# Optimization experiments

Hardware: AMD Instinct MI355X
Metric: run time of the kernel (lower is better)

Reference implementation:

```python
import jax, jax.numpy as jnp
import numpy as np

B, C, IMG, PS, S, D, H, HD, L, OUT = 512, 3, 36, 6, 36, 768, 12, 64, 4, 256

def _pos_embedding(seq_len, dim):
    # NOTE: cos at even indices, sin at odd (as in the torch source)
    position = np.arange(seq_len, dtype=np.float32)[:, None]
    div = np.exp(np.arange(0, dim, 2, dtype=np.float32) * -(np.log(10000.0) / dim))
    emb = np.zeros((seq_len, dim), dtype=np.float32)
    emb[:, 0::2] = np.cos(position * div)
    emb[:, 1::2] = np.sin(position * div)
    return jnp.asarray(emb)

def setup_inputs():
    ks = jax.random.split(jax.random.key(0), 10)
    sc = lambda f: 1.0 / np.sqrt(f)
    return {
        'batch': jax.random.normal(ks[0], (B, C, IMG, IMG), jnp.float32),
        'W_patch': jax.random.normal(ks[1], (D, PS * PS), jnp.float32) * sc(PS * PS),
        'b_patch': jnp.zeros((D,), jnp.float32),
        'pos': _pos_embedding(S, D),
        'ln1_g': jnp.ones((L, D), jnp.float32),
        'ln1_b': jnp.zeros((L, D), jnp.float32),
        'Wq': jax.random.normal(ks[2], (L, H, HD, HD), jnp.float32) * sc(HD),
        'bq': jnp.zeros((L, H, HD), jnp.float32),
        'Wk': jax.random.normal(ks[3], (L, H, HD, HD), jnp.float32) * sc(HD),
        'bk': jnp.zeros((L, H, HD), jnp.float32),
        'Wv': jax.random.normal(ks[4], (L, H, HD, HD), jnp.float32) * sc(HD),
        'bv': jnp.zeros((L, H, HD), jnp.float32),
        'ln2_g': jnp.ones((L, D), jnp.float32),
        'ln2_b': jnp.zeros((L, D), jnp.float32),
        'W1': jax.random.normal(ks[5], (L, 2 * D, D), jnp.float32) * sc(D),
        'b1': jnp.zeros((L, 2 * D), jnp.float32),
        'W2': jax.random.normal(ks[6], (L, D, 2 * D), jnp.float32) * sc(2 * D),
        'b2': jnp.zeros((L, D), jnp.float32),
        'W_out': jax.random.normal(ks[7], (OUT, D), jnp.float32) * sc(D),
        'b_out': jnp.zeros((OUT,), jnp.float32),
    }

def _layernorm(x, g, b):
    m = jnp.mean(x, axis=-1, keepdims=True)
    v = jnp.mean((x - m) ** 2, axis=-1, keepdims=True)
    return (x - m) / jnp.sqrt(v + 1e-5) * g + b

def _forward(batch, W_patch, b_patch, pos, ln1_g, ln1_b, Wq, bq, Wk, bk, Wv, bv,
             ln2_g, ln2_b, W1, b1, W2, b2, W_out, b_out):
    b_, c_ = batch.shape[0], batch.shape[1]
    # patchify: (B,C,36,36) -> (B,C,36 patches,36 pixels), matching torch unfold+reshape
    p = batch.reshape(b_, c_, IMG // PS, PS, IMG // PS, PS)
    p = p.transpose(0, 1, 2, 4, 3, 5).reshape(b_, c_, S, PS * PS)
    z = p @ W_patch.T + b_patch + pos  # pos broadcasts over (B,C)
    scale = 1.0 / np.sqrt(HD)
    for l in range(L):
        # pre-LN then batched per-head attention (collapses the python loops)
        h = _layernorm(z, ln1_g[l], ln1_b[l]).reshape(b_, c_, S, H, HD)
        q = jnp.einsum('bcshd,hed->bcshe', h, Wq[l]) + bq[l]
        k = jnp.einsum('bcshd,hed->bcshe', h, Wk[l]) + bk[l]
        v = jnp.einsum('bcshd,hed->bcshe', h, Wv[l]) + bv[l]
        attn = jax.nn.softmax(jnp.einsum('bcshe,bcthe->bchst', q, k) * scale, axis=-1)
        o = jnp.einsum('bchst,bcthe->bcshe', attn, v).reshape(b_, c_, S, D)
        z = z + o
        z = _layernorm(z, ln2_g[l], ln2_b[l])
        z = z + (jax.nn.relu(z @ W1[l].T + b1[l]) @ W2[l].T + b2[l])
    return z @ W_out.T + b_out

def reference(batch, W_patch, b_patch, pos, ln1_g, ln1_b, Wq, bq, Wk, bk, Wv, bv,
              ln2_g, ln2_b, W1, b1, W2, b2, W_out, b_out):
    return _forward(batch, W_patch, b_patch, pos, ln1_g, ln1_b, Wq, bq, Wk, bk, Wv, bv,
                    ln2_g, ln2_b, W1, b1, W2, b2, W_out, b_out)
```

## Files before the change

### kernel.cpp

```cpp
#include <hip/hip_runtime.h>
#include <hip/hip_bf16.h>
#include <cstdint>
#include <cstddef>

typedef __bf16 bf16;
typedef bf16 bf16x8 __attribute__((ext_vector_type(8)));
typedef bf16 bf16x4 __attribute__((ext_vector_type(4)));
typedef float f32x4 __attribute__((ext_vector_type(4)));
typedef unsigned int u32;

#define GLD_LDS16(gptr, lptr)                                                        \
  __builtin_amdgcn_global_load_lds((const __attribute__((address_space(1))) u32*)(gptr), \
                                   (__attribute__((address_space(3))) u32*)(lptr), 16, 0, 0)

static constexpr int S = 36, D = 768, H = 12, HD = 64, DFF = 1536;
static constexpr int BC = 1536;
static constexpr int M = BC * S;
static constexpr int OUTD = 256;

__global__ __launch_bounds__(256) void f2b_kernel(const float* __restrict__ in,
                                                  bf16* __restrict__ out, int n4) {
  int i = blockIdx.x * 256 + threadIdx.x;
  if (i < n4) {
    float4 f = ((const float4*)in)[i];
    bf16x4 o = {(bf16)f.x, (bf16)f.y, (bf16)f.z, (bf16)f.w};
    ((bf16x4*)out)[i] = o;
  }
}

__global__ __launch_bounds__(256) void patch_embed(const float* __restrict__ batch,
                                                   const float* __restrict__ Wp,
                                                   const float* __restrict__ bp,
                                                   const float* __restrict__ pos,
                                                   float* __restrict__ z) {
  int bc = blockIdx.x, tid = threadIdx.x;
  __shared__ float p[36][40];
  for (int i = tid; i < 1296; i += 256) {
    float f = batch[(size_t)bc * 1296 + i];
    int row = i / 36, col = i - row * 36;
    p[(row / 6) * 6 + col / 6][(row % 6) * 6 + (col % 6)] = f;
  }
  __syncthreads();
  for (int c0 = 0; c0 < 768; c0 += 256) {
    int d = c0 + tid;
    float wr[36];
    const float4* wp4 = (const float4*)(Wp + (size_t)d * 36);
#pragma unroll
    for (int q = 0; q < 9; ++q) {
      float4 f = wp4[q];
      wr[q * 4] = f.x; wr[q * 4 + 1] = f.y; wr[q * 4 + 2] = f.z; wr[q * 4 + 3] = f.w;
    }
    float gb = bp[d];
    for (int s = 0; s < 36; ++s) {
      float acc = 0.f;
#pragma unroll
      for (int k = 0; k < 36; ++k) acc += p[s][k] * wr[k];
      z[((size_t)bc * 36 + s) * 768 + d] = acc + gb + pos[s * 768 + d];
    }
  }
}

__global__ __launch_bounds__(256) void ln_stats(const float* __restrict__ zin,
                                                float* __restrict__ stats) {
  int row = blockIdx.x * 4 + (threadIdx.x >> 6);
  int lane = threadIdx.x & 63;
  const float* zr = zin + (size_t)row * D;
  float x[12];
#pragma unroll
  for (int i = 0; i < 12; ++i) x[i] = zr[i * 64 + lane];
  float s = 0.f;
#pragma unroll
  for (int i = 0; i < 12; ++i) s += x[i];
#pragma unroll
  for (int off = 32; off >= 1; off >>= 1) s += __shfl_xor(s, off, 64);
  float m = s * (1.f / 768.f);
  float v = 0.f;
#pragma unroll
  for (int i = 0; i < 12; ++i) { float dd = x[i] - m; v += dd * dd; }
#pragma unroll
  for (int off = 32; off >= 1; off >>= 1) v += __shfl_xor(v, off, 64);
  v *= (1.f / 768.f);
  if (lane == 0) {
    stats[(size_t)row * 2] = m;
    stats[(size_t)row * 2 + 1] = rsqrtf(v + 1e-5f);
  }
}

__global__ __launch_bounds__(256) void ln_inplace(float* __restrict__ z,
                                                  const float* __restrict__ g,
                                                  const float* __restrict__ bt) {
  int row = blockIdx.x * 4 + (threadIdx.x >> 6);
  int lane = threadIdx.x & 63;
  float* zr = z + (size_t)row * D;
  float x[12];
#pragma unroll
  for (int i = 0; i < 12; ++i) x[i] = zr[i * 64 + lane];
  float s = 0.f;
#pragma unroll
  for (int i = 0; i < 12; ++i) s += x[i];
#pragma unroll
  for (int off = 32; off >= 1; off >>= 1) s += __shfl_xor(s, off, 64);
  float m = s * (1.f / 768.f);
  float v = 0.f;
#pragma unroll
  for (int i = 0; i < 12; ++i) { float dd = x[i] - m; v += dd * dd; }
#pragma unroll
  for (int off = 32; off >= 1; off >>= 1) v += __shfl_xor(v, off, 64);
  v *= (1.f / 768.f);
  float rstd = rsqrtf(v + 1e-5f);
#pragma unroll
  for (int i = 0; i < 12; ++i) {
    int d = i * 64 + lane;
    zr[d] = (x[i] - m) * rstd * g[d] + bt[d];
  }
}

__global__ __launch_bounds__(64) void attn_kernel(const float* __restrict__ zg,
                                                  const float* __restrict__ stats,
                                                  const float* __restrict__ g1,
                                                  const float* __restrict__ b1_,
                                                  const bf16* __restrict__ Wq,
                                                  const bf16* __restrict__ Wk,
                                                  const bf16* __restrict__ Wv,
                                                  const float* __restrict__ bq,
                                                  const float* __restrict__ bk,
                                                  const float* __restrict__ bv,
                                                  float* __restrict__ z) {
  int head = blockIdx.x;
  int bc = blockIdx.y;
  __shared__ __align__(16) bf16 hbuf[48 * 64];
  __shared__ __align__(16) bf16 qbuf[48 * 64];
  __shared__ __align__(16) bf16 kbuf[48 * 64];
  __shared__ __align__(16) bf16 vt[64 * 64];
  __shared__ __align__(16) bf16 pbuf[48 * 64];
  int lane = threadIdx.x;
  int lr = lane & 15, quad = lane >> 4;

  for (int s2 = 36; s2 < 48; ++s2) hbuf[s2 * 64 + lane] = (bf16)0.f;
  for (int i = lane; i < 64 * 16; i += 64) { int e = i >> 4, t = 48 + (i & 15); vt[e * 64 + t] = (bf16)0.f; }
  for (int i = lane; i < 48 * 16; i += 64) { int s2 = i >> 4, t = 48 + (i & 15); pbuf[s2 * 64 + t] = (bf16)0.f; }
  const float* zsrc = zg + ((size_t)bc * S) * D + head * HD;
  const float* st = stats + (size_t)bc * S * 2;
  float gv = g1[head * HD + lane], bvv = b1_[head * HD + lane];
  for (int s2 = 0; s2 < 36; ++s2) {
    float mm = st[s2 * 2], rr = st[s2 * 2 + 1];
    hbuf[s2 * 64 + lane] = (bf16)((zsrc[(size_t)s2 * D + lane] - mm) * rr * gv + bvv);
  }
  __syncthreads();

  const bf16* Wm[3] = {Wq + (size_t)head * 4096, Wk + (size_t)head * 4096, Wv + (size_t)head * 4096};
  const float* Bm[3] = {bq + head * 64, bk + head * 64, bv + head * 64};
  for (int p = 0; p < 3; ++p) {
    bf16x8 bfr[4][2];
#pragma unroll
    for (int nt = 0; nt < 4; ++nt)
#pragma unroll
      for (int kt = 0; kt < 2; ++kt)
        bfr[nt][kt] = *(const bf16x8*)(Wm[p] + (nt * 16 + lr) * 64 + kt * 32 + quad * 8);
#pragma unroll
    for (int mt = 0; mt < 3; ++mt) {
      f32x4 acc[4] = {};
#pragma unroll
      for (int kt = 0; kt < 2; ++kt) {
        bf16x8 a = *(const bf16x8*)&hbuf[(mt * 16 + lr) * 64 + kt * 32 + quad * 8];
#pragma unroll
        for (int nt = 0; nt < 4; ++nt)
          acc[nt] = __builtin_amdgcn_mfma_f32_16x16x32_bf16(a, bfr[nt][kt], acc[nt], 0, 0, 0);
      }
#pragma unroll
      for (int nt = 0; nt < 4; ++nt) {
        float bb = Bm[p][nt * 16 + lr];
#pragma unroll
        for (int r = 0; r < 4; ++r) {
          int s2 = mt * 16 + quad * 4 + r;
          int e = nt * 16 + lr;
          float val = acc[nt][r] + bb;
          if (p == 0) qbuf[s2 * 64 + e] = (bf16)val;
          else if (p == 1) kbuf[s2 * 64 + e] = (bf16)val;
          else vt[e * 64 + s2] = (bf16)val;
        }
      }
    }
  }
  __syncthreads();

  f32x4 sc[3][3];
#pragma unroll
  for (int mt = 0; mt < 3; ++mt)
#pragma unroll
    for (int nt = 0; nt < 3; ++nt) {
      f32x4 a = {};
#pragma unroll
      for (int kt = 0; kt < 2; ++kt) {
        bf16x8 af = *(const bf16x8*)&qbuf[(mt * 16 + lr) * 64 + kt * 32 + quad * 8];
        bf16x8 bf_ = *(const bf16x8*)&kbuf[(nt * 16 + lr) * 64 + kt * 32 + quad * 8];
        a = __builtin_amdgcn_mfma_f32_16x16x32_bf16(af, bf_, a, 0, 0, 0);
      }
      int t = nt * 16 + lr;
#pragma unroll
      for (int r = 0; r < 4; ++r) {
        float v = a[r] * 0.125f;
        if (t >= 36) v = -1e30f;
        sc[mt][nt][r] = v;
      }
    }
#pragma unroll
  for (int mt = 0; mt < 3; ++mt) {
    float mx[4], sum[4];
#pragma unroll
    for (int r = 0; r < 4; ++r)
      mx[r] = fmaxf(fmaxf(sc[mt][0][r], sc[mt][1][r]), sc[mt][2][r]);
#pragma unroll
    for (int r = 0; r < 4; ++r)
#pragma unroll
      for (int off = 8; off >= 1; off >>= 1) mx[r] = fmaxf(mx[r], __shfl_xor(mx[r], off, 64));
#pragma unroll
    for (int r = 0; r < 4; ++r) sum[r] = 0.f;
#pragma unroll
    for (int nt = 0; nt < 3; ++nt)
#pragma unroll
      for (int r = 0; r < 4; ++r) {
        float e = __expf(sc[mt][nt][r] - mx[r]);
        sc[mt][nt][r] = e;
        sum[r] += e;
      }
#pragma unroll
    for (int r = 0; r < 4; ++r)
#pragma unroll
      for (int off = 8; off >= 1; off >>= 1) sum[r] += __shfl_xor(sum[r], off, 64);
#pragma unroll
    for (int nt = 0; nt < 3; ++nt)
#pragma unroll
      for (int r = 0; r < 4; ++r) {
        int s2 = mt * 16 + quad * 4 + r;
        int t = nt * 16 + lr;
        pbuf[s2 * 64 + t] = (bf16)(sc[mt][nt][r] / sum[r]);
      }
  }
  __syncthreads();

#pragma unroll
  for (int mt = 0; mt < 3; ++mt) {
    f32x4 o[4] = {};
#pragma unroll
    for (int kt = 0; kt < 2; ++kt) {
      bf16x8 a = *(const bf16x8*)&pbuf[(mt * 16 + lr) * 64 + kt * 32 + quad * 8];
#pragma unroll
      for (int nt = 0; nt < 4; ++nt) {
        bf16x8 b = *(const bf16x8*)&vt[(nt * 16 + lr) * 64 + kt * 32 + quad * 8];
        o[nt] = __builtin_amdgcn_mfma_f32_16x16x32_bf16(a, b, o[nt], 0, 0, 0);
      }
    }
#pragma unroll
    for (int nt = 0; nt < 4; ++nt)
#pragma unroll
      for (int r = 0; r < 4; ++r) {
        int s2 = mt * 16 + quad * 4 + r;
        if (s2 < 36) {
          int e = nt * 16 + lr;
          size_t idx = ((size_t)bc * S + s2) * D + head * HD + e;
          z[idx] += o[nt][r];
        }
      }
  }
}

template <int N, int K, int MODE, int AF32>
__global__ __launch_bounds__(256) void gemm_bt(const void* __restrict__ A,
                                               const bf16* __restrict__ Bw,
                                               const float* __restrict__ bias,
                                               const float* __restrict__ res,
                                               void* __restrict__ outp) {
  constexpr int BK = 64;
  __shared__ __align__(16) bf16 As[128 * BK];
  __shared__ __align__(16) bf16 Bs[128 * BK];
  int tid = threadIdx.x;
  int bn = blockIdx.x, bm = blockIdx.y;
  const bf16* Abf = (const bf16*)A + (size_t)bm * 128 * K;
  const float* Af = (const float*)A + (size_t)bm * 128 * K;
  const bf16* Bb = Bw + (size_t)bn * 128 * K;
  int lane = tid & 63, wave = tid >> 6;
  int wm = (wave >> 1) * 64, wn = (wave & 1) * 64;
  int lr = lane & 15, quad = lane >> 4;
  f32x4 acc[4][4] = {};
  for (int k0 = 0; k0 < K; k0 += BK) {
    if (AF32) {
#pragma unroll
      for (int r = 0; r < 8; ++r) {
        int c = r * 256 + tid;
        int row = c >> 4, col4 = (c & 15) * 4;
        float4 f = *(const float4*)(Af + (size_t)row * K + k0 + col4);
        bf16x4 o = {(bf16)f.x, (bf16)f.y, (bf16)f.z, (bf16)f.w};
        *(bf16x4*)&As[row * BK + col4] = o;
      }
    } else {
#pragma unroll
      for (int r = 0; r < 4; ++r) {
        int c = r * 256 + tid;
        int row = c >> 3, col = (c & 7) * 8;
        GLD_LDS16(Abf + (size_t)row * K + k0 + col, &As[c * 8]);
      }
    }
#pragma unroll
    for (int r = 0; r < 4; ++r) {
      int c = r * 256 + tid;
      int row = c >> 3, col = (c & 7) * 8;
      GLD_LDS16(Bb + (size_t)row * K + k0 + col, &Bs[c * 8]);
    }
    __syncthreads();
#pragma unroll
    for (int kt = 0; kt < 2; ++kt) {
      bf16x8 af[4], bfr[4];
#pragma unroll
      for (int mt = 0; mt < 4; ++mt) af[mt] = *(const bf16x8*)&As[(wm + mt * 16 + lr) * BK + kt * 32 + quad * 8];
#pragma unroll
      for (int nt = 0; nt < 4; ++nt) bfr[nt] = *(const bf16x8*)&Bs[(wn + nt * 16 + lr) * BK + kt * 32 + quad * 8];
#pragma unroll
      for (int mt = 0; mt < 4; ++mt)
#pragma unroll
        for (int nt = 0; nt < 4; ++nt)
          acc[mt][nt] = __builtin_amdgcn_mfma_f32_16x16x32_bf16(af[mt], bfr[nt], acc[mt][nt], 0, 0, 0);
    }
    __syncthreads();
  }
  int row0 = bm * 128 + wm + quad * 4;
  int col0 = bn * 128 + wn + lr;
#pragma unroll
  for (int mt = 0; mt < 4; ++mt)
#pragma unroll
    for (int nt = 0; nt < 4; ++nt) {
      int col = col0 + nt * 16;
      float bv = bias[col];
#pragma unroll
      for (int r = 0; r < 4; ++r) {
        size_t idx = (size_t)(row0 + mt * 16 + r) * N + col;
        float v = acc[mt][nt][r] + bv;
        if (MODE == 0) ((bf16*)outp)[idx] = (bf16)fmaxf(v, 0.f);
        else if (MODE == 1) ((float*)outp)[idx] = v + res[idx];
        else ((float*)outp)[idx] = v;
      }
    }
}

extern "C" void kernel_launch(void* const* d_in, const int* in_sizes, int n_in,
                              void* d_out, int out_size, void* d_ws, size_t ws_size,
                              hipStream_t stream) {
  const float* batch   = (const float*)d_in[0];
  const float* W_patch = (const float*)d_in[1];
  const float* b_patch = (const float*)d_in[2];
  const float* pos     = (const float*)d_in[3];
  const float* ln1_g   = (const float*)d_in[4];
  const float* ln1_b   = (const float*)d_in[5];
  const float* Wq      = (const float*)d_in[6];
  const float* bq      = (const float*)d_in[7];
  const float* Wk      = (const float*)d_in[8];
  const float* bk      = (const float*)d_in[9];
  const float* Wv      = (const float*)d_in[10];
  const float* bv      = (const float*)d_in[11];
  const float* ln2_g   = (const float*)d_in[12];
  const float* ln2_b   = (const float*)d_in[13];
  const float* W1      = (const float*)d_in[14];
  const float* b1      = (const float*)d_in[15];
  const float* W2      = (const float*)d_in[16];
  const float* b2      = (const float*)d_in[17];
  const float* W_out   = (const float*)d_in[18];
  const float* b_out   = (const float*)d_in[19];
  float* out = (float*)d_out;

  char* ws = (char*)d_ws;
  size_t off = 0;
  float* z     = (float*)(ws + off); off += (size_t)M * D * 4;
  float* stats = (float*)(ws + off); off += (size_t)M * 2 * 4;
  bf16* wq_b = (bf16*)(ws + off);    off += (size_t)4 * H * 4096 * 2;
  bf16* wk_b = (bf16*)(ws + off);    off += (size_t)4 * H * 4096 * 2;
  bf16* wv_b = (bf16*)(ws + off);    off += (size_t)4 * H * 4096 * 2;
  bf16* w1_b = (bf16*)(ws + off);    off += (size_t)4 * DFF * D * 2;
  bf16* w2_b = (bf16*)(ws + off);    off += (size_t)4 * D * DFF * 2;
  bf16* wo_b = (bf16*)(ws + off);    off += (size_t)OUTD * D * 2;
  bf16* act  = (bf16*)(ws + off);

  size_t avail = ws_size > off ? ws_size - off : (size_t)0;
  long long rcl = (long long)(avail / ((size_t)DFF * 2));
  int rc = (rcl > (long long)M) ? M : (int)rcl;
  rc = (rc / 128) * 128;
  if (rc <= 0) rc = 128;

  f2b_kernel<<<192, 256, 0, stream>>>(Wq, wq_b, 49152);
  f2b_kernel<<<192, 256, 0, stream>>>(Wk, wk_b, 49152);
  f2b_kernel<<<192, 256, 0, stream>>>(Wv, wv_b, 49152);
  f2b_kernel<<<4608, 256, 0, stream>>>(W1, w1_b, 1179648);
  f2b_kernel<<<4608, 256, 0, stream>>>(W2, w2_b, 1179648);
  f2b_kernel<<<192, 256, 0, stream>>>(W_out, wo_b, 49152);

  patch_embed<<<BC, 256, 0, stream>>>(batch, W_patch, b_patch, pos, z);

  for (int l = 0; l < 4; ++l) {
    ln_stats<<<M / 4, 256, 0, stream>>>(z, stats);
    attn_kernel<<<dim3(H, BC), 64, 0, stream>>>(z, stats, ln1_g + l * D, ln1_b + l * D,
        wq_b + (size_t)l * H * 4096, wk_b + (size_t)l * H * 4096, wv_b + (size_t)l * H * 4096,
        bq + l * H * 64, bk + l * H * 64, bv + l * H * 64, z);
    ln_inplace<<<M / 4, 256, 0, stream>>>(z, ln2_g + l * D, ln2_b + l * D);
    for (int m0 = 0; m0 < M; m0 += rc) {
      int mr = (M - m0 < rc) ? (M - m0) : rc;
      gemm_bt<DFF, D, 0, 1><<<dim3(DFF / 128, mr / 128), 256, 0, stream>>>(
          z + (size_t)m0 * D, w1_b + (size_t)l * DFF * D, b1 + l * DFF, nullptr, act);
      gemm_bt<D, DFF, 1, 0><<<dim3(D / 128, mr / 128), 256, 0, stream>>>(
          act, w2_b + (size_t)l * D * DFF, b2 + l * D, z + (size_t)m0 * D, z + (size_t)m0 * D);
    }
  }

  gemm_bt<OUTD, D, 2, 1><<<dim3(OUTD / 128, M / 128), 256, 0, stream>>>(
      z, wo_b, b_out, nullptr, out);
}
```

Baseline: 4.019 ms.

## Load LN1 output straight into MFMA fragments and pad attention LDS buffers

The attention kernel now builds the layernormed A fragments for the QKV projection directly in registers using vectorized float4 global loads, instead of staging them through an LDS hbuf. Row strides of the LDS buffers are padded from 64 to 72 to reduce bank conflicts. The probability matrix reuses the Q buffer instead of a separate pbuf, which needs an extra barrier and cuts LDS use, allowing more blocks per CU. The risk is higher register pressure from holding the fragments and gamma/beta values.

```diff
diff --git a/kernel.cpp b/kernel.cpp
--- a/kernel.cpp
+++ b/kernel.cpp
@@ -128,25 +128,59 @@
                                                   float* __restrict__ z) {
   int head = blockIdx.x;
   int bc = blockIdx.y;
-  __shared__ __align__(16) bf16 hbuf[48 * 64];
-  __shared__ __align__(16) bf16 qbuf[48 * 64];
-  __shared__ __align__(16) bf16 kbuf[48 * 64];
-  __shared__ __align__(16) bf16 vt[64 * 64];
-  __shared__ __align__(16) bf16 pbuf[48 * 64];
+  __shared__ __align__(16) bf16 qb[48 * 72];
+  __shared__ __align__(16) bf16 kb[48 * 72];
+  __shared__ __align__(16) bf16 vt[64 * 72];
   int lane = threadIdx.x;
   int lr = lane & 15, quad = lane >> 4;
 
-  for (int s2 = 36; s2 < 48; ++s2) hbuf[s2 * 64 + lane] = (bf16)0.f;
-  for (int i = lane; i < 64 * 16; i += 64) { int e = i >> 4, t = 48 + (i & 15); vt[e * 64 + t] = (bf16)0.f; }
-  for (int i = lane; i < 48 * 16; i += 64) { int s2 = i >> 4, t = 48 + (i & 15); pbuf[s2 * 64 + t] = (bf16)0.f; }
+#pragma unroll
+  for (int t0 = 0; t0 < 16; ++t0) vt[lane * 72 + 48 + t0] = (bf16)0.f;
+
   const float* zsrc = zg + ((size_t)bc * S) * D + head * HD;
   const float* st = stats + (size_t)bc * S * 2;
-  float gv = g1[head * HD + lane], bvv = b1_[head * HD + lane];
-  for (int s2 = 0; s2 < 36; ++s2) {
-    float mm = st[s2 * 2], rr = st[s2 * 2 + 1];
-    hbuf[s2 * 64 + lane] = (bf16)((zsrc[(size_t)s2 * D + lane] - mm) * rr * gv + bvv);
-  }
-  __syncthreads();
+
+  float gv[2][8], bvv[2][8];
+#pragma unroll
+  for (int kt = 0; kt < 2; ++kt) {
+    int c0 = head * HD + kt * 32 + quad * 8;
+    float4 ga = *(const float4*)(g1 + c0);
+    float4 gb2 = *(const float4*)(g1 + c0 + 4);
+    float4 ba = *(const float4*)(b1_ + c0);
+    float4 bb2 = *(const float4*)(b1_ + c0 + 4);
+    gv[kt][0] = ga.x; gv[kt][1] = ga.y; gv[kt][2] = ga.z; gv[kt][3] = ga.w;
+    gv[kt][4] = gb2.x; gv[kt][5] = gb2.y; gv[kt][6] = gb2.z; gv[kt][7] = gb2.w;
+    bvv[kt][0] = ba.x; bvv[kt][1] = ba.y; bvv[kt][2] = ba.z; bvv[kt][3] = ba.w;
+    bvv[kt][4] = bb2.x; bvv[kt][5] = bb2.y; bvv[kt][6] = bb2.z; bvv[kt][7] = bb2.w;
+  }
+
+  bf16x8 hfrag[3][2];
+#pragma unroll
+  for (int mt = 0; mt < 3; ++mt) {
+    int srow = mt * 16 + lr;
+    if (srow < 36) {
+      float mm = st[srow * 2], rr = st[srow * 2 + 1];
+#pragma unroll
+      for (int kt = 0; kt < 2; ++kt) {
+        int c0 = kt * 32 + quad * 8;
+        float4 f0 = *(const float4*)(zsrc + (size_t)srow * D + c0);
+        float4 f1 = *(const float4*)(zsrc + (size_t)srow * D + c0 + 4);
+        float hv[8] = {f0.x, f0.y, f0.z, f0.w, f1.x, f1.y, f1.z, f1.w};
+        bf16x8 o;
+#pragma unroll
+        for (int j = 0; j < 8; ++j) o[j] = (bf16)((hv[j] - mm) * rr * gv[kt][j] + bvv[kt][j]);
+        hfrag[mt][kt] = o;
+      }
+    } else {
+#pragma unroll
+      for (int kt = 0; kt < 2; ++kt) {
+        bf16x8 o;
+#pragma unroll
+        for (int j = 0; j < 8; ++j) o[j] = (bf16)0.f;
+        hfrag[mt][kt] = o;
+      }
+    }
+  }
 
   const bf16* Wm[3] = {Wq + (size_t)head * 4096, Wk + (size_t)head * 4096, Wv + (size_t)head * 4096};
   const float* Bm[3] = {bq + head * 64, bk + head * 64, bv + head * 64};
@@ -161,12 +195,10 @@
     for (int mt = 0; mt < 3; ++mt) {
       f32x4 acc[4] = {};
 #pragma unroll
-      for (int kt = 0; kt < 2; ++kt) {
-        bf16x8 a = *(const bf16x8*)&hbuf[(mt * 16 + lr) * 64 + kt * 32 + quad * 8];
+      for (int kt = 0; kt < 2; ++kt)
 #pragma unroll
         for (int nt = 0; nt < 4; ++nt)
-          acc[nt] = __builtin_amdgcn_mfma_f32_16x16x32_bf16(a, bfr[nt][kt], acc[nt], 0, 0, 0);
-      }
+          acc[nt] = __builtin_amdgcn_mfma_f32_16x16x32_bf16(hfrag[mt][kt], bfr[nt][kt], acc[nt], 0, 0, 0);
 #pragma unroll
       for (int nt = 0; nt < 4; ++nt) {
         float bb = Bm[p][nt * 16 + lr];
@@ -175,9 +207,9 @@
           int s2 = mt * 16 + quad * 4 + r;
           int e = nt * 16 + lr;
           float val = acc[nt][r] + bb;
-          if (p == 0) qbuf[s2 * 64 + e] = (bf16)val;
-          else if (p == 1) kbuf[s2 * 64 + e] = (bf16)val;
-          else vt[e * 64 + s2] = (bf16)val;
+          if (p == 0) qb[s2 * 72 + e] = (bf16)val;
+          else if (p == 1) kb[s2 * 72 + e] = (bf16)val;
+          else vt[e * 72 + s2] = (bf16)val;
         }
       }
     }
@@ -192,8 +224,8 @@
       f32x4 a = {};
 #pragma unroll
       for (int kt = 0; kt < 2; ++kt) {
-        bf16x8 af = *(const bf16x8*)&qbuf[(mt * 16 + lr) * 64 + kt * 32 + quad * 8];
-        bf16x8 bf_ = *(const bf16x8*)&kbuf[(nt * 16 + lr) * 64 + kt * 32 + quad * 8];
+        bf16x8 af = *(const bf16x8*)&qb[(mt * 16 + lr) * 72 + kt * 32 + quad * 8];
+        bf16x8 bf_ = *(const bf16x8*)&kb[(nt * 16 + lr) * 72 + kt * 32 + quad * 8];
         a = __builtin_amdgcn_mfma_f32_16x16x32_bf16(af, bf_, a, 0, 0, 0);
       }
       int t = nt * 16 + lr;
@@ -204,6 +236,8 @@
         sc[mt][nt][r] = v;
       }
     }
+  __syncthreads();
+
 #pragma unroll
   for (int mt = 0; mt < 3; ++mt) {
     float mx[4], sum[4];
@@ -229,12 +263,13 @@
 #pragma unroll
       for (int off = 8; off >= 1; off >>= 1) sum[r] += __shfl_xor(sum[r], off, 64);
 #pragma unroll
-    for (int nt = 0; nt < 3; ++nt)
+    for (int nt = 0; nt < 4; ++nt)
 #pragma unroll
       for (int r = 0; r < 4; ++r) {
         int s2 = mt * 16 + quad * 4 + r;
         int t = nt * 16 + lr;
-        pbuf[s2 * 64 + t] = (bf16)(sc[mt][nt][r] / sum[r]);
+        float pv = (nt < 3) ? sc[mt][nt][r] / sum[r] : 0.f;
+        qb[s2 * 72 + t] = (bf16)pv;
       }
   }
   __syncthreads();
@@ -244,10 +279,10 @@
     f32x4 o[4] = {};
 #pragma unroll
     for (int kt = 0; kt < 2; ++kt) {
-      bf16x8 a = *(const bf16x8*)&pbuf[(mt * 16 + lr) * 64 + kt * 32 + quad * 8];
+      bf16x8 a = *(const bf16x8*)&qb[(mt * 16 + lr) * 72 + kt * 32 + quad * 8];
 #pragma unroll
       for (int nt = 0; nt < 4; ++nt) {
-        bf16x8 b = *(const bf16x8*)&vt[(nt * 16 + lr) * 64 + kt * 32 + quad * 8];
+        bf16x8 b = *(const bf16x8*)&vt[(nt * 16 + lr) * 72 + kt * 32 + quad * 8];
         o[nt] = __builtin_amdgcn_mfma_f32_16x16x32_bf16(a, b, o[nt], 0, 0, 0);
       }
     }
```

Measured after the change: 3.498 ms. -13.0%, faster.
